# Performance work log

Hardware: AMD Instinct MI355X
Metric: run time of the kernel (lower is better)

## Reference

```python
import jax, jax.numpy as jnp
import numpy as np

B, L, DM = 4, 409, 192            # batch, tokens (1 cls + 16 target + 196 template + 196 search), d_model
DI, DS, DR, K, DEPTH = 384, 16, 12, 4, 24   # d_inner=2*DM, d_state, dt_rank=ceil(DM/16), d_conv, depth
EPS = 1e-5


def setup_inputs() -> dict:
    key = jax.random.key(0)
    ks = list(jax.random.split(key, 16))
    def rn(i, shape, s=0.02):
        return jax.random.normal(ks[i], shape, jnp.float32) * s
    # S4D-real init: A = [1..d_state] per channel, stored as log
    A_log = jnp.log(jnp.tile(jnp.arange(1, DS + 1, dtype=jnp.float32), (DEPTH, DI, 1)))
    return {
        "tokens": jax.random.normal(ks[0], (B, L, DM), jnp.float32),
        "norm_w": jnp.ones((DEPTH, DM), jnp.float32),
        "in_proj_w": rn(1, (DEPTH, 2 * DI, DM)),
        "conv_w": rn(2, (DEPTH, DI, 1, K), 0.2),
        "conv_b": jnp.zeros((DEPTH, DI), jnp.float32),
        "conv_w_b": rn(3, (DEPTH, DI, 1, K), 0.2),
        "conv_b_b": jnp.zeros((DEPTH, DI), jnp.float32),
        "x_proj_w": rn(4, (DEPTH, DR + 2 * DS, DI)),
        "x_proj_w_b": rn(5, (DEPTH, DR + 2 * DS, DI)),
        "dt_proj_w": rn(6, (DEPTH, DI, DR), 0.1),
        "dt_bias": rn(7, (DEPTH, DI), 0.5),
        "dt_proj_w_b": rn(8, (DEPTH, DI, DR), 0.1),
        "dt_bias_b": rn(9, (DEPTH, DI), 0.5),
        "A_log": A_log,
        "A_log_b": A_log,
        "D_param": jnp.ones((DEPTH, DI), jnp.float32),
        "D_param_b": jnp.ones((DEPTH, DI), jnp.float32),
        "out_proj_w": rn(10, (DEPTH, DM, DI)),
        "norm_f_w": jnp.ones((DM,), jnp.float32),
    }


def _rms(x, w):
    return x * jax.lax.rsqrt(jnp.mean(x * x, -1, keepdims=True) + EPS) * w


def _causal_conv(x, w, b):
    # x [B,L,DI]; depthwise causal conv1d, kernel K (pad left K-1)
    y = jax.lax.conv_general_dilated(
        jnp.swapaxes(x, 1, 2), w, (1,), [(K - 1, 0)],
        dimension_numbers=("NCH", "OIH", "NCH"), feature_group_count=DI)
    return jnp.swapaxes(y + b[None, :, None], 1, 2)


def _selective_scan(u, delta, A, Bm, Cm, Dp):
    # u,delta [B,L,DI]; A [DI,DS]; Bm,Cm [B,L,DS]; Dp [DI]
    def step(h, inp):
        u_t, d_t, b_t, c_t = inp  # [B,DI],[B,DI],[B,DS],[B,DS]
        h = h * jnp.exp(d_t[..., None] * A) + (d_t * u_t)[..., None] * b_t[:, None, :]
        return h, jnp.einsum("bdn,bn->bd", h, c_t)
    h0 = jnp.zeros((u.shape[0], A.shape[0], A.shape[1]), u.dtype)
    xs = tuple(jnp.swapaxes(t, 0, 1) for t in (u, delta, Bm, Cm))
    _, ys = jax.lax.scan(step, h0, xs)
    return jnp.swapaxes(ys, 0, 1) + u * Dp


def _scan_dir(xin, cw, cb, xpw, dtw, dtb, a_log, dp):
    xf = jax.nn.silu(_causal_conv(xin, cw, cb))
    x_dbl = jnp.einsum("bld,ed->ble", xf, xpw)
    dt, Bm, Cm = jnp.split(x_dbl, [DR, DR + DS], axis=-1)
    dt = jax.nn.softplus(jnp.einsum("blr,dr->bld", dt, dtw) + dtb)
    return _selective_scan(xf, dt, -jnp.exp(a_log), Bm, Cm, dp)


def _mixer(x, p):
    # bimamba v2: forward scan + backward (flipped) scan with separate params
    xz = jnp.einsum("bld,ed->ble", x, p["in_proj_w"])
    xin, z = jnp.split(xz, 2, axis=-1)
    y_f = _scan_dir(xin, p["conv_w"], p["conv_b"], p["x_proj_w"],
                    p["dt_proj_w"], p["dt_bias"], p["A_log"], p["D_param"])
    y_b = _scan_dir(xin[:, ::-1], p["conv_w_b"], p["conv_b_b"], p["x_proj_w_b"],
                    p["dt_proj_w_b"], p["dt_bias_b"], p["A_log_b"], p["D_param_b"])[:, ::-1]
    y = (y_f + y_b) * jax.nn.silu(z) * 0.5   # z-gating + if_divide_out
    return jnp.einsum("ble,de->bld", y, p["out_proj_w"])


def reference(tokens, norm_w, in_proj_w, conv_w, conv_b, conv_w_b, conv_b_b,
              x_proj_w, x_proj_w_b, dt_proj_w, dt_bias, dt_proj_w_b, dt_bias_b,
              A_log, A_log_b, D_param, D_param_b, out_proj_w, norm_f_w):
    stacked = {"norm_w": norm_w, "in_proj_w": in_proj_w,
               "conv_w": conv_w, "conv_b": conv_b, "conv_w_b": conv_w_b, "conv_b_b": conv_b_b,
               "x_proj_w": x_proj_w, "x_proj_w_b": x_proj_w_b,
               "dt_proj_w": dt_proj_w, "dt_bias": dt_bias,
               "dt_proj_w_b": dt_proj_w_b, "dt_bias_b": dt_bias_b,
               "A_log": A_log, "A_log_b": A_log_b,
               "D_param": D_param, "D_param_b": D_param_b,
               "out_proj_w": out_proj_w}

    def layer(carry, p):
        hidden, residual = carry
        residual = residual + hidden          # add (first layer: residual starts at 0)
        h = _rms(residual, p["norm_w"])       # fused_add_norm prenorm path (RMSNorm)
        h = _mixer(h, p)
        return (h, residual), None

    init = (tokens, jnp.zeros_like(tokens))
    (hidden, residual), _ = jax.lax.scan(layer, init, stacked)
    return _rms(residual + hidden, norm_f_w)
```

## Files before the change

kernel.cpp:

```cpp
#include <hip/hip_runtime.h>
#include <math.h>

#define BB     4
#define LLEN   409
#define DMODEL 192
#define DINNER 384
#define DSTATE 16
#define DRANK  12
#define KCONV  4
#define NLAYER 24
#define NROW   (BB*LLEN)
#define EPSF   1e-5f
#define CH2    16
#define NCH2   26

__device__ __forceinline__ float siluf(float x){ return x/(1.f+__expf(-x)); }
__device__ __forceinline__ float softplusf(float x){ return (x>20.f)? x : log1pf(__expf(x)); }

__global__ void k_init(const float* __restrict__ t, float* __restrict__ r, int n){
  int i = blockIdx.x*256+threadIdx.x;
  if (i<n) r[i]=t[i];
}

__global__ __launch_bounds__(256) void k_txp(const float* __restrict__ src,
    float* __restrict__ dst, int R, int C, int RP){
  __shared__ float t[32][33];
  int l = blockIdx.z;
  int c0 = blockIdx.x*32, r0 = blockIdx.y*32;
  const float* s = src + (size_t)l*R*C;
  float* d = dst + (size_t)l*C*RP;
  int tx = threadIdx.x, ty = threadIdx.y;
  #pragma unroll
  for (int yy=ty; yy<32; yy+=8){
    int rr = r0+yy, cc = c0+tx;
    t[yy][tx] = (rr<R && cc<C)? s[(size_t)rr*C+cc] : 0.f;
  }
  __syncthreads();
  #pragma unroll
  for (int yy=ty; yy<32; yy+=8){
    int cc = c0+yy, rr = r0+tx;
    if (cc<C && rr<RP) d[(size_t)cc*RP+rr] = t[tx][yy];
  }
}

__global__ void k_negexpT2(const float* __restrict__ a, float* __restrict__ o, int n){
  int i = blockIdx.x*256+threadIdx.x;
  if (i<n){
    int l = i/(DINNER*DSTATE); int rem = i%(DINNER*DSTATE);
    int nn = rem/DINNER, d = rem%DINNER;
    o[i] = -expf(a[((size_t)l*DINNER + d)*DSTATE + nn]);
  }
}

__global__ __launch_bounds__(256) void k_normin(const float* __restrict__ residual,
    const float* __restrict__ norm_w, const float* __restrict__ Wt,
    float* __restrict__ xz){
  __shared__ __align__(16) float w_lds[192*64];
  __shared__ __align__(16) float a_lds[192*20];
  __shared__ float rs_s[16];
  int tid = threadIdx.x, r0 = blockIdx.x*16, c0 = blockIdx.y*64;
  #pragma unroll
  for (int s=0;s<12;s++){
    int idx = tid + s*256; int i = idx/DMODEL, k = idx%DMODEL; int row = r0+i;
    a_lds[k*20+i] = (row<NROW)? residual[(size_t)row*DMODEL+k] : 0.f;
  }
  {
    int j4 = (tid&15)*4, kr = tid>>4;
    #pragma unroll
    for (int s=0;s<12;s++){
      int k = kr + s*16;
      *reinterpret_cast<float4*>(&w_lds[k*64+j4]) =
        *reinterpret_cast<const float4*>(&Wt[(size_t)k*768 + c0 + j4]);
    }
  }
  __syncthreads();
  int wv = tid>>6, lane = tid&63;
  {
    float ss[4] = {0.f,0.f,0.f,0.f};
    #pragma unroll
    for (int q=0;q<3;q++){
      int k = lane + q*64;
      #pragma unroll
      for (int r=0;r<4;r++){ float v = a_lds[k*20 + wv*4 + r]; ss[r] += v*v; }
    }
    #pragma unroll
    for (int r=0;r<4;r++){
      float s = ss[r];
      #pragma unroll
      for (int off=1; off<64; off<<=1) s += __shfl_xor(s, off, 64);
      if (lane==0) rs_s[wv*4+r] = rsqrtf(s/(float)DMODEL + EPSF);
    }
  }
  __syncthreads();
  #pragma unroll
  for (int s=0;s<12;s++){
    int idx = tid + s*256; int k = idx>>4, i = idx&15;
    a_lds[k*20+i] *= rs_s[i]*norm_w[k];
  }
  __syncthreads();
  int j = tid & 63, rg = tid >> 6;
  float acc[4] = {0.f,0.f,0.f,0.f};
  #pragma unroll 8
  for (int k=0;k<192;k++){
    float w = w_lds[k*64+j];
    float4 a = *reinterpret_cast<const float4*>(&a_lds[k*20 + rg*4]);
    acc[0]+=a.x*w; acc[1]+=a.y*w; acc[2]+=a.z*w; acc[3]+=a.w*w;
  }
  #pragma unroll
  for (int q=0;q<4;q++){
    int row = r0 + rg*4 + q;
    if (row<NROW) xz[(size_t)row*768 + c0 + j] = acc[q];
  }
}

__global__ __launch_bounds__(256) void k_conv(const float* __restrict__ xz,
    const float* __restrict__ cwf, const float* __restrict__ cbf,
    const float* __restrict__ cwb, const float* __restrict__ cbb,
    float* __restrict__ xf_f, float* __restrict__ xf_b){
  int idx = blockIdx.x*256 + threadIdx.x;
  if (idx >= NROW*(DINNER/4)) return;
  int d4 = (idx % (DINNER/4))*4; int bl = idx / (DINNER/4);
  int b = bl / LLEN; int l = bl % LLEN;
  int dir = blockIdx.y;
  const float* cw = dir? cwb : cwf;
  const float* cb = dir? cbb : cbf;
  float4 w0 = *reinterpret_cast<const float4*>(&cw[(d4+0)*KCONV]);
  float4 w1 = *reinterpret_cast<const float4*>(&cw[(d4+1)*KCONV]);
  float4 w2 = *reinterpret_cast<const float4*>(&cw[(d4+2)*KCONV]);
  float4 w3 = *reinterpret_cast<const float4*>(&cw[(d4+3)*KCONV]);
  float4 acc = *reinterpret_cast<const float4*>(&cb[d4]);
  const float* wa0 = (const float*)&w0; const float* wa1 = (const float*)&w1;
  const float* wa2 = (const float*)&w2; const float* wa3 = (const float*)&w3;
  #pragma unroll
  for (int k=0;k<KCONV;k++){
    int o = dir? (LLEN-1-l-k+3) : (l-3+k);
    bool ok = dir? (l+k>=3) : (o>=0);
    if (ok){
      float4 x = *reinterpret_cast<const float4*>(&xz[((size_t)(b*LLEN+o))*768 + d4]);
      acc.x += wa0[k]*x.x; acc.y += wa1[k]*x.y; acc.z += wa2[k]*x.z; acc.w += wa3[k]*x.w;
    }
  }
  float* out = dir? xf_b : xf_f;
  float4 r; r.x = siluf(acc.x); r.y = siluf(acc.y); r.z = siluf(acc.z); r.w = siluf(acc.w);
  *reinterpret_cast<float4*>(&out[(size_t)bl*DINNER + d4]) = r;
}

__global__ __launch_bounds__(256) void k_xp2(
    const float* __restrict__ xf_f, const float* __restrict__ xf_b,
    const float* __restrict__ WxpPF, const float* __restrict__ WxpPB,
    const float* __restrict__ WdtF, const float* __restrict__ WdtB,
    const float* __restrict__ dtbF, const float* __restrict__ dtbB,
    float* __restrict__ dtbc_f, float* __restrict__ dtbc_b,
    float* __restrict__ dt_f, float* __restrict__ dt_b){
  __shared__ __align__(16) float w_lds[192*64];
  __shared__ __align__(16) float a_lds[192*20];
  __shared__ float dtin_s[16*12];
  int dir = blockIdx.z;
  const float* xf  = dir? xf_b : xf_f;
  const float* Wxp = dir? WxpPB : WxpPF;
  const float* Wdt = dir? WdtB : WdtF;
  const float* dtb = dir? dtbB : dtbF;
  float* dtbc = dir? dtbc_b : dtbc_f;
  float* dtp  = dir? dt_b  : dt_f;
  int tid = threadIdx.x, r0 = blockIdx.x*16;
  int j = tid & 63, rg = tid >> 6;
  float acc[4] = {0.f,0.f,0.f,0.f};
  for (int c=0;c<2;c++){
    int K0 = c*192;
    if (c) __syncthreads();
    {
      int j4 = (tid&15)*4, kr = tid>>4;
      #pragma unroll
      for (int s=0;s<12;s++){
        int k = kr + s*16;
        *reinterpret_cast<float4*>(&w_lds[k*64+j4]) =
          *reinterpret_cast<const float4*>(&Wxp[(size_t)(K0+k)*64 + j4]);
      }
    }
    {
      int i = tid>>4, kc = (tid&15)*12;
      int row = r0+i;
      #pragma unroll
      for (int m=0;m<12;m+=4){
        float4 v = make_float4(0.f,0.f,0.f,0.f);
        if (row<NROW) v = *reinterpret_cast<const float4*>(&xf[(size_t)row*DINNER + K0 + kc + m]);
        a_lds[(kc+m+0)*20+i]=v.x; a_lds[(kc+m+1)*20+i]=v.y;
        a_lds[(kc+m+2)*20+i]=v.z; a_lds[(kc+m+3)*20+i]=v.w;
      }
    }
    __syncthreads();
    #pragma unroll 8
    for (int k=0;k<192;k++){
      float w = w_lds[k*64+j];
      float4 a = *reinterpret_cast<const float4*>(&a_lds[k*20 + rg*4]);
      acc[0]+=a.x*w; acc[1]+=a.y*w; acc[2]+=a.z*w; acc[3]+=a.w*w;
    }
  }
  __syncthreads();
  #pragma unroll
  for (int q=0;q<4;q++){
    int i = rg*4+q, row = r0+i;
    if (j<44 && row<NROW) dtbc[(size_t)row*44 + j] = acc[q];
    if (j<12) dtin_s[i*12 + j] = acc[q];
  }
  __syncthreads();
  for (int idx=tid; idx<12*DINNER; idx+=256) w_lds[idx] = Wdt[idx];
  __syncthreads();
  for (int idx=tid; idx<16*DINNER; idx+=256){
    int i = idx/DINNER, dd = idx - i*DINNER;
    int row = r0+i;
    float v = dtb[dd];
    #pragma unroll
    for (int r=0;r<12;r++) v += dtin_s[i*12+r]*w_lds[r*DINNER+dd];
    if (row<NROW) dtp[(size_t)row*DINNER+dd] = softplusf(v);
  }
}

__global__ __launch_bounds__(128) void k_scan1(
    const float* __restrict__ xf_f, const float* __restrict__ xf_b,
    const float* __restrict__ dtbc_f, const float* __restrict__ dtbc_b,
    const float* __restrict__ dt_f, const float* __restrict__ dt_b,
    const float* __restrict__ anF, const float* __restrict__ anB,
    float* __restrict__ q_buf, float* __restrict__ sdt_buf){
  int dir = blockIdx.z;
  int b  = blockIdx.y / NCH2;
  int ch = blockIdx.y % NCH2;
  const float* xf   = dir? xf_b  : xf_f;
  const float* dtbc = dir? dtbc_b: dtbc_f;
  const float* dtp  = dir? dt_b  : dt_f;
  const float* an   = dir? anB   : anF;
  int t0 = ch*CH2;
  int T  = (t0+CH2<=LLEN)? CH2 : (LLEN-t0);
  int d0 = blockIdx.x*128;
  size_t base = (size_t)b*LLEN + t0;
  __shared__ float dt_s[CH2*128], u_s[CH2*128];
  __shared__ __align__(16) float B_s[CH2*16];
  int tid = threadIdx.x;
  for (int t=0;t<T;t++){
    dt_s[t*128+tid] = dtp[(base+t)*DINNER + d0 + tid];
    u_s [t*128+tid] = xf [(base+t)*DINNER + d0 + tid];
  }
  for (int idx = tid; idx < T*16; idx += 128){
    int t = idx>>4, n = idx&15;
    B_s[idx] = dtbc[(base+t)*44 + 12 + n];
  }
  __syncthreads();
  int d = d0 + tid;
  float A[16], h[16];
  #pragma unroll
  for (int n=0;n<16;n++){ A[n] = an[n*DINNER + d]; h[n] = 0.f; }
  float sdt = 0.f;
  for (int t=0;t<T;t++){
    float dtv = dt_s[t*128+tid];
    float du  = dtv * u_s[t*128+tid];
    float Bv[16];
    #pragma unroll
    for (int q=0;q<4;q++) *reinterpret_cast<float4*>(&Bv[q*4]) =
        *reinterpret_cast<const float4*>(&B_s[t*16 + q*4]);
    #pragma unroll
    for (int n=0;n<16;n++) h[n] = h[n]*__expf(dtv*A[n]) + du*Bv[n];
    sdt += dtv;
  }
  size_t ci = ((size_t)dir*BB + b)*NCH2 + ch;
  float* qo = &q_buf[(ci*DINNER + d)*DSTATE];
  #pragma unroll
  for (int q=0;q<4;q++) *reinterpret_cast<float4*>(&qo[q*4]) =
      make_float4(h[q*4+0], h[q*4+1], h[q*4+2], h[q*4+3]);
  sdt_buf[ci*DINNER + d] = sdt;
}

__global__ __launch_bounds__(256) void k_carry(
    const float* __restrict__ anF, const float* __restrict__ anB,
    float* __restrict__ q_buf, const float* __restrict__ sdt_buf){
  int g = blockIdx.x*256 + threadIdx.x;
  int n = g & 15; int r1 = g >> 4;
  int d = r1 % DINNER; int r2 = r1 / DINNER;
  int b = r2 & 3; int dir = r2 >> 2;
  const float* an = dir? anB : anF;
  float A = an[n*DINNER + d];
  size_t sbase = ((size_t)dir*BB + b)*NCH2;
  float h = 0.f;
  for (int cc=0; cc<NCH2; cc++){
    size_t qi = ((sbase+cc)*DINNER + d)*DSTATE + n;
    float qv = q_buf[qi];
    float sv = sdt_buf[(sbase+cc)*DINNER + d];
    q_buf[qi] = h;
    h = qv + __expf(A*sv)*h;
  }
}

__global__ __launch_bounds__(128) void k_scan2(
    const float* __restrict__ xf_f, const float* __restrict__ xf_b,
    const float* __restrict__ dtbc_f, const float* __restrict__ dtbc_b,
    const float* __restrict__ dt_f, const float* __restrict__ dt_b,
    const float* __restrict__ anF, const float* __restrict__ anB,
    const float* __restrict__ DpF, const float* __restrict__ DpB,
    const float* __restrict__ q_buf,
    float* __restrict__ y_fo, float* __restrict__ y_bo){
  int dir = blockIdx.z;
  int b  = blockIdx.y / NCH2;
  int ch = blockIdx.y % NCH2;
  const float* xf   = dir? xf_b  : xf_f;
  const float* dtbc = dir? dtbc_b: dtbc_f;
  const float* dtp  = dir? dt_b  : dt_f;
  const float* an   = dir? anB   : anF;
  const float* Dp   = dir? DpB   : DpF;
  float* y = dir? y_bo : y_fo;
  int t0 = ch*CH2;
  int T  = (t0+CH2<=LLEN)? CH2 : (LLEN-t0);
  int d0 = blockIdx.x*128;
  size_t base = (size_t)b*LLEN + t0;
  __shared__ float dt_s[CH2*128], u_s[CH2*128];
  __shared__ __align__(16) float B_s[CH2*16], C_s[CH2*16];
  int tid = threadIdx.x;
  for (int t=0;t<T;t++){
    dt_s[t*128+tid] = dtp[(base+t)*DINNER + d0 + tid];
    u_s [t*128+tid] = xf [(base+t)*DINNER + d0 + tid];
  }
  for (int idx = tid; idx < T*16; idx += 128){
    int t = idx>>4, n = idx&15;
    B_s[idx] = dtbc[(base+t)*44 + 12 + n];
    C_s[idx] = dtbc[(base+t)*44 + 28 + n];
  }
  __syncthreads();
  int d = d0 + tid;
  size_t ci = ((size_t)dir*BB + b)*NCH2 + ch;
  const float* qi = &q_buf[(ci*DINNER + d)*DSTATE];
  float A[16], h[16];
  #pragma unroll
  for (int q=0;q<4;q++){
    float4 hv = *reinterpret_cast<const float4*>(&qi[q*4]);
    h[q*4+0]=hv.x; h[q*4+1]=hv.y; h[q*4+2]=hv.z; h[q*4+3]=hv.w;
  }
  #pragma unroll
  for (int n=0;n<16;n++) A[n] = an[n*DINNER + d];
  float Dd = Dp[d];
  for (int t=0;t<T;t++){
    float dtv = dt_s[t*128+tid];
    float u   = u_s [t*128+tid];
    float du  = dtv*u;
    float Bv[16], Cv[16];
    #pragma unroll
    for (int q=0;q<4;q++){
      *reinterpret_cast<float4*>(&Bv[q*4]) = *reinterpret_cast<const float4*>(&B_s[t*16+q*4]);
      *reinterpret_cast<float4*>(&Cv[q*4]) = *reinterpret_cast<const float4*>(&C_s[t*16+q*4]);
    }
    float y0=0.f, y1=0.f, y2=0.f, y3=0.f;
    #pragma unroll
    for (int n=0;n<16;n+=4){
      h[n+0] = h[n+0]*__expf(dtv*A[n+0]) + du*Bv[n+0];
      h[n+1] = h[n+1]*__expf(dtv*A[n+1]) + du*Bv[n+1];
      h[n+2] = h[n+2]*__expf(dtv*A[n+2]) + du*Bv[n+2];
      h[n+3] = h[n+3]*__expf(dtv*A[n+3]) + du*Bv[n+3];
      y0 += h[n+0]*Cv[n+0]; y1 += h[n+1]*Cv[n+1];
      y2 += h[n+2]*Cv[n+2]; y3 += h[n+3]*Cv[n+3];
    }
    y[(base+t)*DINNER + d] = (y0+y1)+(y2+y3) + u*Dd;
  }
}

__global__ __launch_bounds__(256) void k_gateout(
    const float* __restrict__ y_f, const float* __restrict__ y_b,
    const float* __restrict__ xz, const float* __restrict__ Wt,
    float* __restrict__ residual){
  __shared__ __align__(16) float w_lds[192*64];
  __shared__ __align__(16) float a_lds[192*20];
  int tid = threadIdx.x, r0 = blockIdx.x*16, c0 = blockIdx.y*64;
  int j = tid & 63, rg = tid >> 6;
  float acc[4] = {0.f,0.f,0.f,0.f};
  for (int c=0;c<2;c++){
    int K0 = c*192;
    if (c) __syncthreads();
    {
      int j4 = (tid&15)*4, kr = tid>>4;
      #pragma unroll
      for (int s=0;s<12;s++){
        int k = kr + s*16;
        *reinterpret_cast<float4*>(&w_lds[k*64+j4]) =
          *reinterpret_cast<const float4*>(&Wt[(size_t)(K0+k)*192 + c0 + j4]);
      }
    }
    #pragma unroll
    for (int s=0;s<12;s++){
      int idx = tid + s*256; int i = idx/192, k = idx - i*192;
      int row = r0+i; float v = 0.f;
      if (row<NROW){
        int b = row/LLEN, l = row - b*LLEN;
        int rrow = b*LLEN + (LLEN-1-l);
        float yf = y_f[(size_t)row*DINNER + K0 + k];
        float yb = y_b[(size_t)rrow*DINNER + K0 + k];
        float z  = xz[(size_t)row*768 + DINNER + K0 + k];
        v = (yf+yb)*siluf(z)*0.5f;
      }
      a_lds[k*20+i] = v;
    }
    __syncthreads();
    #pragma unroll 8
    for (int k=0;k<192;k++){
      float w = w_lds[k*64+j];
      float4 a = *reinterpret_cast<const float4*>(&a_lds[k*20 + rg*4]);
      acc[0]+=a.x*w; acc[1]+=a.y*w; acc[2]+=a.z*w; acc[3]+=a.w*w;
    }
  }
  #pragma unroll
  for (int q=0;q<4;q++){
    int row = r0 + rg*4 + q;
    if (row<NROW) residual[(size_t)row*DMODEL + c0 + j] += acc[q];
  }
}

__global__ __launch_bounds__(256) void k_final(const float* __restrict__ residual,
    const float* __restrict__ nfw, float* __restrict__ out){
  int wv = threadIdx.x>>6, lane = threadIdx.x&63;
  int row = blockIdx.x*4 + wv;
  if (row >= NROW) return;
  float v[3]; float s = 0.f;
  #pragma unroll
  for (int q=0;q<3;q++){ v[q] = residual[(size_t)row*DMODEL + lane + q*64]; s += v[q]*v[q]; }
  #pragma unroll
  for (int off=1; off<64; off<<=1) s += __shfl_xor(s, off, 64);
  float sc = rsqrtf(s/(float)DMODEL + EPSF);
  #pragma unroll
  for (int q=0;q<3;q++) out[(size_t)row*DMODEL + lane + q*64] = v[q]*sc*nfw[lane + q*64];
}

extern "C" void kernel_launch(void* const* d_in, const int* in_sizes, int n_in,
                              void* d_out, int out_size, void* d_ws, size_t ws_size,
                              hipStream_t stream){
  const float* tokens     = (const float*)d_in[0];
  const float* norm_w     = (const float*)d_in[1];
  const float* in_proj_w  = (const float*)d_in[2];
  const float* conv_w     = (const float*)d_in[3];
  const float* conv_b     = (const float*)d_in[4];
  const float* conv_w_b   = (const float*)d_in[5];
  const float* conv_b_b   = (const float*)d_in[6];
  const float* x_proj_w   = (const float*)d_in[7];
  const float* x_proj_w_b = (const float*)d_in[8];
  const float* dt_proj_w  = (const float*)d_in[9];
  const float* dt_bias    = (const float*)d_in[10];
  const float* dt_proj_w_b= (const float*)d_in[11];
  const float* dt_bias_b  = (const float*)d_in[12];
  const float* A_log      = (const float*)d_in[13];
  const float* A_log_b    = (const float*)d_in[14];
  const float* D_param    = (const float*)d_in[15];
  const float* D_param_b  = (const float*)d_in[16];
  const float* out_proj_w = (const float*)d_in[17];
  const float* norm_f_w   = (const float*)d_in[18];

  float* ws = (float*)d_ws;
  size_t off = 0;
  float* residual = ws + off; off += (size_t)NROW*DMODEL;
  float* xz       = ws + off; off += (size_t)NROW*768;
  float* xf_f     = ws + off; off += (size_t)NROW*DINNER;
  float* xf_b     = ws + off; off += (size_t)NROW*DINNER;
  float* dtbc_f   = ws + off; off += (size_t)NROW*44;
  float* dtbc_b   = ws + off; off += (size_t)NROW*44;
  float* dt_f     = ws + off; off += (size_t)NROW*DINNER;
  float* dt_b     = ws + off; off += (size_t)NROW*DINNER;
  float* y_f      = ws + off; off += (size_t)NROW*DINNER;
  float* y_b      = ws + off; off += (size_t)NROW*DINNER;
  float* q_buf    = ws + off; off += (size_t)2*BB*NCH2*DINNER*DSTATE;
  float* sdt_buf  = ws + off; off += (size_t)2*BB*NCH2*DINNER;
  float* WtIn     = ws + off; off += (size_t)NLAYER*DMODEL*768;
  float* WtXpPF   = ws + off; off += (size_t)NLAYER*DINNER*64;
  float* WtXpPB   = ws + off; off += (size_t)NLAYER*DINNER*64;
  float* WtDtF    = ws + off; off += (size_t)NLAYER*DRANK*DINNER;
  float* WtDtB    = ws + off; off += (size_t)NLAYER*DRANK*DINNER;
  float* WtOut    = ws + off; off += (size_t)NLAYER*DINNER*DMODEL;
  float* AnTF     = ws + off; off += (size_t)NLAYER*DINNER*DSTATE;
  float* AnTB     = ws + off; off += (size_t)NLAYER*DINNER*DSTATE;
  if (off*sizeof(float) > ws_size) return;

  k_init<<<dim3((NROW*DMODEL+255)/256),256,0,stream>>>(tokens, residual, NROW*DMODEL);
  dim3 tb(32,8);
  k_txp<<<dim3(6,24,NLAYER),tb,0,stream>>>(in_proj_w,  WtIn,   768, 192, 768);
  k_txp<<<dim3(12,2,NLAYER),tb,0,stream>>>(x_proj_w,   WtXpPF,  44, 384,  64);
  k_txp<<<dim3(12,2,NLAYER),tb,0,stream>>>(x_proj_w_b, WtXpPB,  44, 384,  64);
  k_txp<<<dim3(1,12,NLAYER),tb,0,stream>>>(dt_proj_w,  WtDtF,  384,  12, 384);
  k_txp<<<dim3(1,12,NLAYER),tb,0,stream>>>(dt_proj_w_b,WtDtB,  384,  12, 384);
  k_txp<<<dim3(12,6,NLAYER),tb,0,stream>>>(out_proj_w, WtOut,  192, 384, 192);
  k_negexpT2<<<dim3((NLAYER*DINNER*DSTATE+255)/256),256,0,stream>>>(A_log,   AnTF, NLAYER*DINNER*DSTATE);
  k_negexpT2<<<dim3((NLAYER*DINNER*DSTATE+255)/256),256,0,stream>>>(A_log_b, AnTB, NLAYER*DINNER*DSTATE);

  const int RT16 = (NROW+15)/16;
  const int EW4  = (NROW*(DINNER/4)+255)/256;
  for (int l=0; l<NLAYER; l++){
    k_normin<<<dim3(RT16,12),256,0,stream>>>(residual, norm_w + (size_t)l*DMODEL,
        WtIn + (size_t)l*DMODEL*768, xz);
    k_conv<<<dim3(EW4,2),256,0,stream>>>(xz,
        conv_w + (size_t)l*DINNER*KCONV, conv_b + (size_t)l*DINNER,
        conv_w_b + (size_t)l*DINNER*KCONV, conv_b_b + (size_t)l*DINNER, xf_f, xf_b);
    k_xp2<<<dim3(RT16,1,2),256,0,stream>>>(xf_f, xf_b,
        WtXpPF + (size_t)l*DINNER*64, WtXpPB + (size_t)l*DINNER*64,
        WtDtF + (size_t)l*DRANK*DINNER, WtDtB + (size_t)l*DRANK*DINNER,
        dt_bias + (size_t)l*DINNER, dt_bias_b + (size_t)l*DINNER,
        dtbc_f, dtbc_b, dt_f, dt_b);
    k_scan1<<<dim3(3,BB*NCH2,2),128,0,stream>>>(xf_f, xf_b, dtbc_f, dtbc_b, dt_f, dt_b,
        AnTF + (size_t)l*DINNER*DSTATE, AnTB + (size_t)l*DINNER*DSTATE, q_buf, sdt_buf);
    k_carry<<<dim3(192),256,0,stream>>>(
        AnTF + (size_t)l*DINNER*DSTATE, AnTB + (size_t)l*DINNER*DSTATE, q_buf, sdt_buf);
    k_scan2<<<dim3(3,BB*NCH2,2),128,0,stream>>>(xf_f, xf_b, dtbc_f, dtbc_b, dt_f, dt_b,
        AnTF + (size_t)l*DINNER*DSTATE, AnTB + (size_t)l*DINNER*DSTATE,
        D_param + (size_t)l*DINNER, D_param_b + (size_t)l*DINNER,
        q_buf, y_f, y_b);
    k_gateout<<<dim3(RT16,3),256,0,stream>>>(y_f, y_b, xz, WtOut + (size_t)l*DINNER*DMODEL, residual);
  }
  k_final<<<dim3((NROW+3)/4),256,0,stream>>>(residual, norm_f_w, (float*)d_out);
}
```

Measured before the change: 2.824 ms.

## Fuse per-layer kernels into a persistent cooperative megakernel with grid syncs

Replaces the 7 kernel launches per layer with one cooperative persistent kernel that loops over layers and phases, separated by grid-wide barriers. The separate carry kernel is removed: each scan2 block now rebuilds its incoming state by serially combining the chunk summaries of all earlier chunks. The aim is to cut launch overhead and inter-kernel gaps across 24 layers. In exchange, the grid is capped at 512 blocks, grid.sync costs are added, and scan2 does redundant carry work that grows with the chunk index. A fallback path with normal launches remains.

```diff
diff --git a/kernel.cpp b/kernel.cpp
--- a/kernel.cpp
+++ b/kernel.cpp
@@ -1,5 +1,8 @@
 #include <hip/hip_runtime.h>
+#include <hip/hip_cooperative_groups.h>
 #include <math.h>
+
+namespace cg = cooperative_groups;
 
 #define BB     4
 #define LLEN   409
@@ -14,8 +17,28 @@
 #define CH2    16
 #define NCH2   26
 
+#define OFF_A    12288
+#define OFF_RS   16128
+#define OFF_DTIN 16144
+#define SMEMF    16336
+
+#define NT_NORMIN  1236
+#define NT_CONV    (2*NROW*96)
+#define NT_XP2     206
+#define NT_SCANP   312
+#define NT_GATEOUT 309
+
 __device__ __forceinline__ float siluf(float x){ return x/(1.f+__expf(-x)); }
 __device__ __forceinline__ float softplusf(float x){ return (x>20.f)? x : log1pf(__expf(x)); }
+
+struct MP {
+  const float *norm_w, *conv_w, *conv_b, *conv_w_b, *conv_b_b;
+  const float *dt_bias, *dt_bias_b, *D_param, *D_param_b, *norm_f_w;
+  float *residual, *xz, *xf_f, *xf_b, *dtbc_f, *dtbc_b, *dt_f, *dt_b, *y_f, *y_b;
+  float *q_buf, *sdt_buf;
+  float *WtIn, *WtXpPF, *WtXpPB, *WtDtF, *WtDtB, *WtOut, *AnTF, *AnTB;
+  float *out;
+};
 
 __global__ void k_init(const float* __restrict__ t, float* __restrict__ r, int n){
   int i = blockIdx.x*256+threadIdx.x;
@@ -52,17 +75,18 @@
   }
 }
 
-__global__ __launch_bounds__(256) void k_normin(const float* __restrict__ residual,
-    const float* __restrict__ norm_w, const float* __restrict__ Wt,
-    float* __restrict__ xz){
-  __shared__ __align__(16) float w_lds[192*64];
-  __shared__ __align__(16) float a_lds[192*20];
-  __shared__ float rs_s[16];
-  int tid = threadIdx.x, r0 = blockIdx.x*16, c0 = blockIdx.y*64;
+__device__ void ph_normin(float* sm, int task, int l, const MP& P){
+  float* w_lds = sm;
+  float* a_lds = sm + OFF_A;
+  float* rs_s  = sm + OFF_RS;
+  const float* norm_w = P.norm_w + (size_t)l*DMODEL;
+  const float* Wt     = P.WtIn   + (size_t)l*DMODEL*768;
+  int tid = threadIdx.x;
+  int r0 = (task/12)*16, c0 = (task%12)*64;
   #pragma unroll
   for (int s=0;s<12;s++){
     int idx = tid + s*256; int i = idx/DMODEL, k = idx%DMODEL; int row = r0+i;
-    a_lds[k*20+i] = (row<NROW)? residual[(size_t)row*DMODEL+k] : 0.f;
+    a_lds[k*20+i] = (row<NROW)? P.residual[(size_t)row*DMODEL+k] : 0.f;
   }
   {
     int j4 = (tid&15)*4, kr = tid>>4;
@@ -109,21 +133,18 @@
   #pragma unroll
   for (int q=0;q<4;q++){
     int row = r0 + rg*4 + q;
-    if (row<NROW) xz[(size_t)row*768 + c0 + j] = acc[q];
-  }
-}
-
-__global__ __launch_bounds__(256) void k_conv(const float* __restrict__ xz,
-    const float* __restrict__ cwf, const float* __restrict__ cbf,
-    const float* __restrict__ cwb, const float* __restrict__ cbb,
-    float* __restrict__ xf_f, float* __restrict__ xf_b){
-  int idx = blockIdx.x*256 + threadIdx.x;
-  if (idx >= NROW*(DINNER/4)) return;
-  int d4 = (idx % (DINNER/4))*4; int bl = idx / (DINNER/4);
-  int b = bl / LLEN; int l = bl % LLEN;
-  int dir = blockIdx.y;
-  const float* cw = dir? cwb : cwf;
-  const float* cb = dir? cbb : cbf;
+    if (row<NROW) P.xz[(size_t)row*768 + c0 + j] = acc[q];
+  }
+  __syncthreads();
+}
+
+__device__ void ph_conv(int i, int l, const MP& P){
+  int dir = i / (NROW*96);
+  int rem = i - dir*(NROW*96);
+  int d4 = (rem % 96)*4; int bl = rem / 96;
+  int b = bl / LLEN; int ll = bl % LLEN;
+  const float* cw = (dir? P.conv_w_b : P.conv_w) + (size_t)l*DINNER*KCONV;
+  const float* cb = (dir? P.conv_b_b : P.conv_b) + (size_t)l*DINNER;
   float4 w0 = *reinterpret_cast<const float4*>(&cw[(d4+0)*KCONV]);
   float4 w1 = *reinterpret_cast<const float4*>(&cw[(d4+1)*KCONV]);
   float4 w2 = *reinterpret_cast<const float4*>(&cw[(d4+2)*KCONV]);
@@ -133,36 +154,30 @@
   const float* wa2 = (const float*)&w2; const float* wa3 = (const float*)&w3;
   #pragma unroll
   for (int k=0;k<KCONV;k++){
-    int o = dir? (LLEN-1-l-k+3) : (l-3+k);
-    bool ok = dir? (l+k>=3) : (o>=0);
+    int o = dir? (LLEN-1-ll-k+3) : (ll-3+k);
+    bool ok = dir? (ll+k>=3) : (o>=0);
     if (ok){
-      float4 x = *reinterpret_cast<const float4*>(&xz[((size_t)(b*LLEN+o))*768 + d4]);
+      float4 x = *reinterpret_cast<const float4*>(&P.xz[((size_t)(b*LLEN+o))*768 + d4]);
       acc.x += wa0[k]*x.x; acc.y += wa1[k]*x.y; acc.z += wa2[k]*x.z; acc.w += wa3[k]*x.w;
     }
   }
-  float* out = dir? xf_b : xf_f;
+  float* out = dir? P.xf_b : P.xf_f;
   float4 r; r.x = siluf(acc.x); r.y = siluf(acc.y); r.z = siluf(acc.z); r.w = siluf(acc.w);
   *reinterpret_cast<float4*>(&out[(size_t)bl*DINNER + d4]) = r;
 }
 
-__global__ __launch_bounds__(256) void k_xp2(
-    const float* __restrict__ xf_f, const float* __restrict__ xf_b,
-    const float* __restrict__ WxpPF, const float* __restrict__ WxpPB,
-    const float* __restrict__ WdtF, const float* __restrict__ WdtB,
-    const float* __restrict__ dtbF, const float* __restrict__ dtbB,
-    float* __restrict__ dtbc_f, float* __restrict__ dtbc_b,
-    float* __restrict__ dt_f, float* __restrict__ dt_b){
-  __shared__ __align__(16) float w_lds[192*64];
-  __shared__ __align__(16) float a_lds[192*20];
-  __shared__ float dtin_s[16*12];
-  int dir = blockIdx.z;
-  const float* xf  = dir? xf_b : xf_f;
-  const float* Wxp = dir? WxpPB : WxpPF;
-  const float* Wdt = dir? WdtB : WdtF;
-  const float* dtb = dir? dtbB : dtbF;
-  float* dtbc = dir? dtbc_b : dtbc_f;
-  float* dtp  = dir? dt_b  : dt_f;
-  int tid = threadIdx.x, r0 = blockIdx.x*16;
+__device__ void ph_xp2(float* sm, int task, int l, const MP& P){
+  float* w_lds  = sm;
+  float* a_lds  = sm + OFF_A;
+  float* dtin_s = sm + OFF_DTIN;
+  int dir = task & 1, rt = task >> 1;
+  const float* xf  = dir? P.xf_b : P.xf_f;
+  const float* Wxp = (dir? P.WtXpPB : P.WtXpPF) + (size_t)l*DINNER*64;
+  const float* Wdt = (dir? P.WtDtB  : P.WtDtF ) + (size_t)l*DRANK*DINNER;
+  const float* dtb = (dir? P.dt_bias_b : P.dt_bias) + (size_t)l*DINNER;
+  float* dtbc = dir? P.dtbc_b : P.dtbc_f;
+  float* dtp  = dir? P.dt_b   : P.dt_f;
+  int tid = threadIdx.x, r0 = rt*16;
   int j = tid & 63, rg = tid >> 6;
   float acc[4] = {0.f,0.f,0.f,0.f};
   for (int c=0;c<2;c++){
@@ -214,45 +229,44 @@
     for (int r=0;r<12;r++) v += dtin_s[i*12+r]*w_lds[r*DINNER+dd];
     if (row<NROW) dtp[(size_t)row*DINNER+dd] = softplusf(v);
   }
-}
-
-__global__ __launch_bounds__(128) void k_scan1(
-    const float* __restrict__ xf_f, const float* __restrict__ xf_b,
-    const float* __restrict__ dtbc_f, const float* __restrict__ dtbc_b,
-    const float* __restrict__ dt_f, const float* __restrict__ dt_b,
-    const float* __restrict__ anF, const float* __restrict__ anB,
-    float* __restrict__ q_buf, float* __restrict__ sdt_buf){
-  int dir = blockIdx.z;
-  int b  = blockIdx.y / NCH2;
-  int ch = blockIdx.y % NCH2;
-  const float* xf   = dir? xf_b  : xf_f;
-  const float* dtbc = dir? dtbc_b: dtbc_f;
-  const float* dtp  = dir? dt_b  : dt_f;
-  const float* an   = dir? anB   : anF;
+  __syncthreads();
+}
+
+__device__ void ph_scan1(float* sm, int pair, int l, const MP& P){
+  int tid = threadIdx.x;
+  int sub = tid>>7, ltid = tid&127;
+  int gt  = pair*2 + sub;
+  int dir = gt / 312; int rem = gt % 312;
+  int bch = rem / 3;  int d0b = rem % 3;
+  int b = bch / NCH2, ch = bch % NCH2;
+  const float* xf   = dir? P.xf_b  : P.xf_f;
+  const float* dtbc = dir? P.dtbc_b: P.dtbc_f;
+  const float* dtp  = dir? P.dt_b  : P.dt_f;
+  const float* an   = (dir? P.AnTB : P.AnTF) + (size_t)l*DINNER*DSTATE;
   int t0 = ch*CH2;
   int T  = (t0+CH2<=LLEN)? CH2 : (LLEN-t0);
-  int d0 = blockIdx.x*128;
+  int d0 = d0b*128;
   size_t base = (size_t)b*LLEN + t0;
-  __shared__ float dt_s[CH2*128], u_s[CH2*128];
-  __shared__ __align__(16) float B_s[CH2*16];
-  int tid = threadIdx.x;
+  float* dt_s = sm + sub*5120;
+  float* u_s  = dt_s + 2048;
+  float* B_s  = dt_s + 4096;
   for (int t=0;t<T;t++){
-    dt_s[t*128+tid] = dtp[(base+t)*DINNER + d0 + tid];
-    u_s [t*128+tid] = xf [(base+t)*DINNER + d0 + tid];
-  }
-  for (int idx = tid; idx < T*16; idx += 128){
+    dt_s[t*128+ltid] = dtp[(base+t)*DINNER + d0 + ltid];
+    u_s [t*128+ltid] = xf [(base+t)*DINNER + d0 + ltid];
+  }
+  for (int idx = ltid; idx < T*16; idx += 128){
     int t = idx>>4, n = idx&15;
     B_s[idx] = dtbc[(base+t)*44 + 12 + n];
   }
   __syncthreads();
-  int d = d0 + tid;
+  int d = d0 + ltid;
   float A[16], h[16];
   #pragma unroll
   for (int n=0;n<16;n++){ A[n] = an[n*DINNER + d]; h[n] = 0.f; }
   float sdt = 0.f;
   for (int t=0;t<T;t++){
-    float dtv = dt_s[t*128+tid];
-    float du  = dtv * u_s[t*128+tid];
+    float dtv = dt_s[t*128+ltid];
+    float du  = dtv * u_s[t*128+ltid];
     float Bv[16];
     #pragma unroll
     for (int q=0;q<4;q++) *reinterpret_cast<float4*>(&Bv[q*4]) =
@@ -262,82 +276,60 @@
     sdt += dtv;
   }
   size_t ci = ((size_t)dir*BB + b)*NCH2 + ch;
-  float* qo = &q_buf[(ci*DINNER + d)*DSTATE];
+  float* qo = &P.q_buf[(ci*DINNER + d)*DSTATE];
   #pragma unroll
   for (int q=0;q<4;q++) *reinterpret_cast<float4*>(&qo[q*4]) =
       make_float4(h[q*4+0], h[q*4+1], h[q*4+2], h[q*4+3]);
-  sdt_buf[ci*DINNER + d] = sdt;
-}
-
-__global__ __launch_bounds__(256) void k_carry(
-    const float* __restrict__ anF, const float* __restrict__ anB,
-    float* __restrict__ q_buf, const float* __restrict__ sdt_buf){
-  int g = blockIdx.x*256 + threadIdx.x;
-  int n = g & 15; int r1 = g >> 4;
-  int d = r1 % DINNER; int r2 = r1 / DINNER;
-  int b = r2 & 3; int dir = r2 >> 2;
-  const float* an = dir? anB : anF;
-  float A = an[n*DINNER + d];
-  size_t sbase = ((size_t)dir*BB + b)*NCH2;
-  float h = 0.f;
-  for (int cc=0; cc<NCH2; cc++){
-    size_t qi = ((sbase+cc)*DINNER + d)*DSTATE + n;
-    float qv = q_buf[qi];
-    float sv = sdt_buf[(sbase+cc)*DINNER + d];
-    q_buf[qi] = h;
-    h = qv + __expf(A*sv)*h;
-  }
-}
-
-__global__ __launch_bounds__(128) void k_scan2(
-    const float* __restrict__ xf_f, const float* __restrict__ xf_b,
-    const float* __restrict__ dtbc_f, const float* __restrict__ dtbc_b,
-    const float* __restrict__ dt_f, const float* __restrict__ dt_b,
-    const float* __restrict__ anF, const float* __restrict__ anB,
-    const float* __restrict__ DpF, const float* __restrict__ DpB,
-    const float* __restrict__ q_buf,
-    float* __restrict__ y_fo, float* __restrict__ y_bo){
-  int dir = blockIdx.z;
-  int b  = blockIdx.y / NCH2;
-  int ch = blockIdx.y % NCH2;
-  const float* xf   = dir? xf_b  : xf_f;
-  const float* dtbc = dir? dtbc_b: dtbc_f;
-  const float* dtp  = dir? dt_b  : dt_f;
-  const float* an   = dir? anB   : anF;
-  const float* Dp   = dir? DpB   : DpF;
-  float* y = dir? y_bo : y_fo;
+  P.sdt_buf[ci*DINNER + d] = sdt;
+  __syncthreads();
+}
+
+__device__ void ph_scan2(float* sm, int pair, int l, const MP& P){
+  int tid = threadIdx.x;
+  int sub = tid>>7, ltid = tid&127;
+  int gt  = pair*2 + sub;
+  int dir = gt / 312; int rem = gt % 312;
+  int bch = rem / 3;  int d0b = rem % 3;
+  int b = bch / NCH2, ch = bch % NCH2;
+  const float* xf   = dir? P.xf_b  : P.xf_f;
+  const float* dtbc = dir? P.dtbc_b: P.dtbc_f;
+  const float* dtp  = dir? P.dt_b  : P.dt_f;
+  const float* an   = (dir? P.AnTB : P.AnTF) + (size_t)l*DINNER*DSTATE;
+  const float* Dp   = (dir? P.D_param_b : P.D_param) + (size_t)l*DINNER;
+  float* y = dir? P.y_b : P.y_f;
   int t0 = ch*CH2;
   int T  = (t0+CH2<=LLEN)? CH2 : (LLEN-t0);
-  int d0 = blockIdx.x*128;
+  int d0 = d0b*128;
   size_t base = (size_t)b*LLEN + t0;
-  __shared__ float dt_s[CH2*128], u_s[CH2*128];
-  __shared__ __align__(16) float B_s[CH2*16], C_s[CH2*16];
-  int tid = threadIdx.x;
+  float* dt_s = sm + sub*5120;
+  float* u_s  = dt_s + 2048;
+  float* B_s  = dt_s + 4096;
+  float* C_s  = dt_s + 4352;
   for (int t=0;t<T;t++){
-    dt_s[t*128+tid] = dtp[(base+t)*DINNER + d0 + tid];
-    u_s [t*128+tid] = xf [(base+t)*DINNER + d0 + tid];
-  }
-  for (int idx = tid; idx < T*16; idx += 128){
+    dt_s[t*128+ltid] = dtp[(base+t)*DINNER + d0 + ltid];
+    u_s [t*128+ltid] = xf [(base+t)*DINNER + d0 + ltid];
+  }
+  for (int idx = ltid; idx < T*16; idx += 128){
     int t = idx>>4, n = idx&15;
     B_s[idx] = dtbc[(base+t)*44 + 12 + n];
     C_s[idx] = dtbc[(base+t)*44 + 28 + n];
   }
   __syncthreads();
-  int d = d0 + tid;
-  size_t ci = ((size_t)dir*BB + b)*NCH2 + ch;
-  const float* qi = &q_buf[(ci*DINNER + d)*DSTATE];
+  int d = d0 + ltid;
   float A[16], h[16];
   #pragma unroll
-  for (int q=0;q<4;q++){
-    float4 hv = *reinterpret_cast<const float4*>(&qi[q*4]);
-    h[q*4+0]=hv.x; h[q*4+1]=hv.y; h[q*4+2]=hv.z; h[q*4+3]=hv.w;
-  }
-  #pragma unroll
-  for (int n=0;n<16;n++) A[n] = an[n*DINNER + d];
+  for (int n=0;n<16;n++){ A[n] = an[n*DINNER + d]; h[n] = 0.f; }
+  size_t sbase = ((size_t)dir*BB + b)*NCH2;
+  for (int cc=0; cc<ch; cc++){
+    float sv = P.sdt_buf[(sbase+cc)*DINNER + d];
+    const float* qp = &P.q_buf[((sbase+cc)*DINNER + d)*DSTATE];
+    #pragma unroll
+    for (int n=0;n<16;n++) h[n] = qp[n] + __expf(A[n]*sv)*h[n];
+  }
   float Dd = Dp[d];
   for (int t=0;t<T;t++){
-    float dtv = dt_s[t*128+tid];
-    float u   = u_s [t*128+tid];
+    float dtv = dt_s[t*128+ltid];
+    float u   = u_s [t*128+ltid];
     float du  = dtv*u;
     float Bv[16], Cv[16];
     #pragma unroll
@@ -357,15 +349,15 @@
     }
     y[(base+t)*DINNER + d] = (y0+y1)+(y2+y3) + u*Dd;
   }
-}
-
-__global__ __launch_bounds__(256) void k_gateout(
-    const float* __restrict__ y_f, const float* __restrict__ y_b,
-    const float* __restrict__ xz, const float* __restrict__ Wt,
-    float* __restrict__ residual){
-  __shared__ __align__(16) float w_lds[192*64];
-  __shared__ __align__(16) float a_lds[192*20];
-  int tid = threadIdx.x, r0 = blockIdx.x*16, c0 = blockIdx.y*64;
+  __syncthreads();
+}
+
+__device__ void ph_gateout(float* sm, int task, int l, const MP& P){
+  float* w_lds = sm;
+  float* a_lds = sm + OFF_A;
+  const float* Wt = P.WtOut + (size_t)l*DINNER*DMODEL;
+  int tid = threadIdx.x;
+  int r0 = (task/3)*16, c0 = (task%3)*64;
   int j = tid & 63, rg = tid >> 6;
   float acc[4] = {0.f,0.f,0.f,0.f};
   for (int c=0;c<2;c++){
@@ -385,11 +377,11 @@
       int idx = tid + s*256; int i = idx/192, k = idx - i*192;
       int row = r0+i; float v = 0.f;
       if (row<NROW){
-        int b = row/LLEN, l = row - b*LLEN;
-        int rrow = b*LLEN + (LLEN-1-l);
-        float yf = y_f[(size_t)row*DINNER + K0 + k];
-        float yb = y_b[(size_t)rrow*DINNER + K0 + k];
-        float z  = xz[(size_t)row*768 + DINNER + K0 + k];
+        int b = row/LLEN, ll = row - b*LLEN;
+        int rrow = b*LLEN + (LLEN-1-ll);
+        float yf = P.y_f[(size_t)row*DINNER + K0 + k];
+        float yb = P.y_b[(size_t)rrow*DINNER + K0 + k];
+        float z  = P.xz[(size_t)row*768 + DINNER + K0 + k];
         v = (yf+yb)*siluf(z)*0.5f;
       }
       a_lds[k*20+i] = v;
@@ -405,23 +397,69 @@
   #pragma unroll
   for (int q=0;q<4;q++){
     int row = r0 + rg*4 + q;
-    if (row<NROW) residual[(size_t)row*DMODEL + c0 + j] += acc[q];
-  }
-}
-
-__global__ __launch_bounds__(256) void k_final(const float* __restrict__ residual,
-    const float* __restrict__ nfw, float* __restrict__ out){
-  int wv = threadIdx.x>>6, lane = threadIdx.x&63;
-  int row = blockIdx.x*4 + wv;
-  if (row >= NROW) return;
+    if (row<NROW) P.residual[(size_t)row*DMODEL + c0 + j] += acc[q];
+  }
+  __syncthreads();
+}
+
+__device__ void ph_final(int row, const MP& P){
+  int lane = threadIdx.x&63;
   float v[3]; float s = 0.f;
   #pragma unroll
-  for (int q=0;q<3;q++){ v[q] = residual[(size_t)row*DMODEL + lane + q*64]; s += v[q]*v[q]; }
+  for (int q=0;q<3;q++){ v[q] = P.residual[(size_t)row*DMODEL + lane + q*64]; s += v[q]*v[q]; }
   #pragma unroll
   for (int off=1; off<64; off<<=1) s += __shfl_xor(s, off, 64);
   float sc = rsqrtf(s/(float)DMODEL + EPSF);
   #pragma unroll
-  for (int q=0;q<3;q++) out[(size_t)row*DMODEL + lane + q*64] = v[q]*sc*nfw[lane + q*64];
+  for (int q=0;q<3;q++) P.out[(size_t)row*DMODEL + lane + q*64] = v[q]*sc*P.norm_f_w[lane + q*64];
+}
+
+__global__ __launch_bounds__(256) void k_mega(MP P){
+  cg::grid_group gg = cg::this_grid();
+  __shared__ float sm[SMEMF];
+  int nb = gridDim.x, bid = blockIdx.x, tid = threadIdx.x;
+  for (int l=0; l<NLAYER; l++){
+    for (int t=bid; t<NT_NORMIN; t+=nb) ph_normin(sm, t, l, P);
+    gg.sync();
+    for (int i=bid*256+tid; i<NT_CONV; i+=nb*256) ph_conv(i, l, P);
+    gg.sync();
+    for (int t=bid; t<NT_XP2; t+=nb) ph_xp2(sm, t, l, P);
+    gg.sync();
+    for (int t=bid; t<NT_SCANP; t+=nb) ph_scan1(sm, t, l, P);
+    gg.sync();
+    for (int t=bid; t<NT_SCANP; t+=nb) ph_scan2(sm, t, l, P);
+    gg.sync();
+    for (int t=bid; t<NT_GATEOUT; t+=nb) ph_gateout(sm, t, l, P);
+    gg.sync();
+  }
+  for (int r = bid*4 + (tid>>6); r < NROW; r += nb*4) ph_final(r, P);
+}
+
+__global__ __launch_bounds__(256) void kw_normin(MP P, int l){
+  __shared__ float sm[SMEMF];
+  for (int t=blockIdx.x; t<NT_NORMIN; t+=gridDim.x) ph_normin(sm, t, l, P);
+}
+__global__ __launch_bounds__(256) void kw_conv(MP P, int l){
+  for (int i=blockIdx.x*256+threadIdx.x; i<NT_CONV; i+=gridDim.x*256) ph_conv(i, l, P);
+}
+__global__ __launch_bounds__(256) void kw_xp2(MP P, int l){
+  __shared__ float sm[SMEMF];
+  for (int t=blockIdx.x; t<NT_XP2; t+=gridDim.x) ph_xp2(sm, t, l, P);
+}
+__global__ __launch_bounds__(256) void kw_scan1(MP P, int l){
+  __shared__ float sm[SMEMF];
+  for (int t=blockIdx.x; t<NT_SCANP; t+=gridDim.x) ph_scan1(sm, t, l, P);
+}
+__global__ __launch_bounds__(256) void kw_scan2(MP P, int l){
+  __shared__ float sm[SMEMF];
+  for (int t=blockIdx.x; t<NT_SCANP; t+=gridDim.x) ph_scan2(sm, t, l, P);
+}
+__global__ __launch_bounds__(256) void kw_gateout(MP P, int l){
+  __shared__ float sm[SMEMF];
+  for (int t=blockIdx.x; t<NT_GATEOUT; t+=gridDim.x) ph_gateout(sm, t, l, P);
+}
+__global__ __launch_bounds__(256) void kw_final(MP P){
+  for (int r = blockIdx.x*4 + (threadIdx.x>>6); r < NROW; r += gridDim.x*4) ph_final(r, P);
 }
 
 extern "C" void kernel_launch(void* const* d_in, const int* in_sizes, int n_in,
@@ -482,28 +520,44 @@
   k_negexpT2<<<dim3((NLAYER*DINNER*DSTATE+255)/256),256,0,stream>>>(A_log,   AnTF, NLAYER*DINNER*DSTATE);
   k_negexpT2<<<dim3((NLAYER*DINNER*DSTATE+255)/256),256,0,stream>>>(A_log_b, AnTB, NLAYER*DINNER*DSTATE);
 
-  const int RT16 = (NROW+15)/16;
-  const int EW4  = (NROW*(DINNER/4)+255)/256;
-  for (int l=0; l<NLAYER; l++){
-    k_normin<<<dim3(RT16,12),256,0,stream>>>(residual, norm_w + (size_t)l*DMODEL,
-        WtIn + (size_t)l*DMODEL*768, xz);
-    k_conv<<<dim3(EW4,2),256,0,stream>>>(xz,
-        conv_w + (size_t)l*DINNER*KCONV, conv_b + (size_t)l*DINNER,
-        conv_w_b + (size_t)l*DINNER*KCONV, conv_b_b + (size_t)l*DINNER, xf_f, xf_b);
-    k_xp2<<<dim3(RT16,1,2),256,0,stream>>>(xf_f, xf_b,
-        WtXpPF + (size_t)l*DINNER*64, WtXpPB + (size_t)l*DINNER*64,
-        WtDtF + (size_t)l*DRANK*DINNER, WtDtB + (size_t)l*DRANK*DINNER,
-        dt_bias + (size_t)l*DINNER, dt_bias_b + (size_t)l*DINNER,
-        dtbc_f, dtbc_b, dt_f, dt_b);
-    k_scan1<<<dim3(3,BB*NCH2,2),128,0,stream>>>(xf_f, xf_b, dtbc_f, dtbc_b, dt_f, dt_b,
-        AnTF + (size_t)l*DINNER*DSTATE, AnTB + (size_t)l*DINNER*DSTATE, q_buf, sdt_buf);
-    k_carry<<<dim3(192),256,0,stream>>>(
-        AnTF + (size_t)l*DINNER*DSTATE, AnTB + (size_t)l*DINNER*DSTATE, q_buf, sdt_buf);
-    k_scan2<<<dim3(3,BB*NCH2,2),128,0,stream>>>(xf_f, xf_b, dtbc_f, dtbc_b, dt_f, dt_b,
-        AnTF + (size_t)l*DINNER*DSTATE, AnTB + (size_t)l*DINNER*DSTATE,
-        D_param + (size_t)l*DINNER, D_param_b + (size_t)l*DINNER,
-        q_buf, y_f, y_b);
-    k_gateout<<<dim3(RT16,3),256,0,stream>>>(y_f, y_b, xz, WtOut + (size_t)l*DINNER*DMODEL, residual);
-  }
-  k_final<<<dim3((NROW+3)/4),256,0,stream>>>(residual, norm_f_w, (float*)d_out);
-}
+  MP P;
+  P.norm_w = norm_w; P.conv_w = conv_w; P.conv_b = conv_b;
+  P.conv_w_b = conv_w_b; P.conv_b_b = conv_b_b;
+  P.dt_bias = dt_bias; P.dt_bias_b = dt_bias_b;
+  P.D_param = D_param; P.D_param_b = D_param_b; P.norm_f_w = norm_f_w;
+  P.residual = residual; P.xz = xz; P.xf_f = xf_f; P.xf_b = xf_b;
+  P.dtbc_f = dtbc_f; P.dtbc_b = dtbc_b; P.dt_f = dt_f; P.dt_b = dt_b;
+  P.y_f = y_f; P.y_b = y_b; P.q_buf = q_buf; P.sdt_buf = sdt_buf;
+  P.WtIn = WtIn; P.WtXpPF = WtXpPF; P.WtXpPB = WtXpPB;
+  P.WtDtF = WtDtF; P.WtDtB = WtDtB; P.WtOut = WtOut;
+  P.AnTF = AnTF; P.AnTB = AnTB;
+  P.out = (float*)d_out;
+
+  int coopOK = 0;
+  int dev = 0; hipGetDevice(&dev);
+  hipDeviceProp_t prop;
+  if (hipGetDeviceProperties(&prop, dev) == hipSuccess && prop.cooperativeLaunch){
+    int maxb = 0;
+    if (hipOccupancyMaxActiveBlocksPerMultiprocessor(&maxb, k_mega, 256, 0) == hipSuccess && maxb > 0){
+      int nblk = maxb * prop.multiProcessorCount;
+      if (nblk > 512) nblk = 512;
+      if (nblk >= 64){
+        void* args[] = { (void*)&P };
+        hipError_t e = hipLaunchCooperativeKernel((const void*)k_mega,
+            dim3(nblk), dim3(256), args, 0, stream);
+        if (e == hipSuccess) coopOK = 1;
+      }
+    }
+  }
+  if (!coopOK){
+    for (int l=0; l<NLAYER; l++){
+      kw_normin <<<dim3(NT_NORMIN),256,0,stream>>>(P, l);
+      kw_conv   <<<dim3((NT_CONV+255)/256),256,0,stream>>>(P, l);
+      kw_xp2    <<<dim3(NT_XP2),256,0,stream>>>(P, l);
+      kw_scan1  <<<dim3(NT_SCANP),256,0,stream>>>(P, l);
+      kw_scan2  <<<dim3(NT_SCANP),256,0,stream>>>(P, l);
+      kw_gateout<<<dim3(NT_GATEOUT),256,0,stream>>>(P, l);
+    }
+    kw_final<<<dim3((NROW+3)/4),256,0,stream>>>(P);
+  }
+}
```

Measured after the change: 2.844 ms. About the same (+0.7%).
